# Performance work log

Measured on AMD Instinct MI355X. Metric: run time of the kernel, lower is better.

## Reference

```python
import jax, jax.numpy as jnp
import numpy as np

DIM = 512
NUM_HEADS = 16
HEAD_DIM = DIM // NUM_HEADS
HIDDEN = int(DIM * 4.0)
EPS = 1e-5


def layer_norm(x, gamma, beta):
    mu = jnp.mean(x, axis=-1, keepdims=True)
    var = jnp.mean(jnp.square(x - mu), axis=-1, keepdims=True)
    return (x - mu) * jax.lax.rsqrt(var + EPS) * gamma + beta


def setup_inputs() -> dict:
    key = jax.random.key(0)
    ks = jax.random.split(key, 8)
    B, L, C = 32, 3136, DIM
    x = jax.random.normal(ks[0], (B, L, C), dtype=jnp.float32)
    norm1_g = jnp.ones((C,), jnp.float32)
    norm1_b = jnp.zeros((C,), jnp.float32)
    # spatial (per-head) mixing weight: (num_heads, head_dim, head_dim)
    w_spatial = jax.random.normal(ks[1], (NUM_HEADS, HEAD_DIM, HEAD_DIM), jnp.float32) * (1.0 / np.sqrt(HEAD_DIM))
    norm2_g = jnp.ones((C,), jnp.float32)
    norm2_b = jnp.zeros((C,), jnp.float32)
    w1 = jax.random.normal(ks[2], (C, HIDDEN), jnp.float32) * (1.0 / np.sqrt(C))
    b1 = jnp.zeros((HIDDEN,), jnp.float32)
    w2 = jax.random.normal(ks[3], (HIDDEN, C), jnp.float32) * (1.0 / np.sqrt(HIDDEN))
    b2 = jnp.zeros((C,), jnp.float32)
    return {"x": x, "norm1_g": norm1_g, "norm1_b": norm1_b, "w_spatial": w_spatial,
            "norm2_g": norm2_g, "norm2_b": norm2_b, "w1": w1, "b1": b1, "w2": w2, "b2": b2}


def reference(x, norm1_g, norm1_b, w_spatial, norm2_g, norm2_b, w1, b1, w2, b2):
    B, L, C = x.shape
    shortcut = x
    h = layer_norm(x, norm1_g, norm1_b)
    # window partition -> per-head channel-sub-dim linear (shared across windows/positions)
    # mathematically equivalent to applying the per-head matmul at every token
    h = h.reshape(B, L, NUM_HEADS, HEAD_DIM)
    h = jnp.einsum('blhd,hde->blhe', h, w_spatial)
    h = h.reshape(B, L, C)
    x = shortcut + h
    # channel MLP: Linear -> GELU(tanh) -> Linear
    y = layer_norm(x, norm2_g, norm2_b)
    y = jax.nn.gelu(y @ w1 + b1, approximate=True)
    y = y @ w2 + b2
    return x + y
```

## Files before the change

kernel.cpp:

```cpp
#include <hip/hip_runtime.h>
#include <hip/hip_bf16.h>


typedef __bf16 bf16x8 __attribute__((ext_vector_type(8)));
typedef float f32x4 __attribute__((ext_vector_type(4)));

constexpr int CDIM = 512;
constexpr int HID = 2048;
constexpr int MROWS = 32 * 3136;
constexpr float LN_EPS = 1e-5f;

static __device__ __forceinline__ float gelu_tanh(float x) {
  const float u = 0.7978845608028654f * fmaf(0.044715f * x * x, x, x);
  const float e = __expf(2.0f * u);
  return 0.5f * x * (2.0f - 2.0f / (e + 1.0f));
}

static __device__ __forceinline__ void load_lds16(const void* g, void* l) {
  __builtin_amdgcn_global_load_lds((__attribute__((address_space(1))) void*)g,
                                   (__attribute__((address_space(3))) void*)l,
                                   16, 0, 0);
}

template <int KD, int ND>
__global__ __launch_bounds__(256) void cvt_t(const float* __restrict__ src,
                                             __hip_bfloat16* __restrict__ dst) {
  __shared__ float tl[64][65];
  const int t = threadIdx.x;
  constexpr int NTN = ND / 64;
  const int k0 = (blockIdx.x / NTN) * 64;
  const int n0 = (blockIdx.x % NTN) * 64;
  const int c4 = (t & 15) * 4;
  const int r = t >> 4;
#pragma unroll
  for (int j = 0; j < 4; ++j) {
    const int kk = r + j * 16;
    const float4 v = *(const float4*)&src[(size_t)(k0 + kk) * ND + n0 + c4];
    tl[c4 + 0][kk] = v.x;
    tl[c4 + 1][kk] = v.y;
    tl[c4 + 2][kk] = v.z;
    tl[c4 + 3][kk] = v.w;
  }
  __syncthreads();
#pragma unroll
  for (int j = 0; j < 4; ++j) {
    const int nn = r + j * 16;
    __hip_bfloat16 o[4];
#pragma unroll
    for (int c = 0; c < 4; ++c) o[c] = __float2bfloat16(tl[nn][c4 + c]);
    *(uint2*)&dst[(size_t)(n0 + nn) * KD + k0 + c4] = *(const uint2*)o;
  }
}

__global__ __launch_bounds__(256) void fused_pre(
    const float* __restrict__ x, const float* __restrict__ g1,
    const float* __restrict__ b1, const float* __restrict__ wsp,
    const float* __restrict__ g2, const float* __restrict__ b2,
    float* __restrict__ x2out, __hip_bfloat16* __restrict__ yout) {
  __shared__ float lnbuf[CDIM];
  __shared__ float red[8];

  const int t = threadIdx.x;
  const int lane = t & 63;
  const int w = t >> 6;
  const int c0 = 2 * t;
  const int hd = c0 >> 5, e0 = c0 & 31;

  float wc0[32], wc1[32];
#pragma unroll
  for (int d = 0; d < 32; ++d) {
    const float2 wv = *(const float2*)&wsp[(hd * 32 + d) * 32 + e0];
    wc0[d] = wv.x;
    wc1[d] = wv.y;
  }
  const float2 g1v = *(const float2*)&g1[c0];
  const float2 b1v = *(const float2*)&b1[c0];
  const float2 g2v = *(const float2*)&g2[c0];
  const float2 b2v = *(const float2*)&b2[c0];

  for (int r = blockIdx.x; r < MROWS; r += gridDim.x) {
    const float2 xv = *(const float2*)&x[(size_t)r * CDIM + c0];

    float s = xv.x + xv.y, ss = xv.x * xv.x + xv.y * xv.y;
#pragma unroll
    for (int off = 32; off; off >>= 1) {
      s += __shfl_down(s, off);
      ss += __shfl_down(ss, off);
    }
    if (lane == 0) { red[w * 2] = s; red[w * 2 + 1] = ss; }
    __syncthreads();
    s = red[0] + red[2] + red[4] + red[6];
    ss = red[1] + red[3] + red[5] + red[7];
    float mu = s * (1.0f / CDIM);
    float var = ss * (1.0f / CDIM) - mu * mu;
    float rs = rsqrtf(var + LN_EPS);
    lnbuf[c0] = (xv.x - mu) * rs * g1v.x + b1v.x;
    lnbuf[c0 + 1] = (xv.y - mu) * rs * g1v.y + b1v.y;
    __syncthreads();

    float h0 = 0.f, h1 = 0.f;
#pragma unroll
    for (int d = 0; d < 32; ++d) {
      const float lv = lnbuf[hd * 32 + d];
      h0 = fmaf(lv, wc0[d], h0);
      h1 = fmaf(lv, wc1[d], h1);
    }
    const float a0 = xv.x + h0, a1 = xv.y + h1;
    float2 av;
    av.x = a0;
    av.y = a1;
    *(float2*)&x2out[(size_t)r * CDIM + c0] = av;

    s = a0 + a1;
    ss = a0 * a0 + a1 * a1;
#pragma unroll
    for (int off = 32; off; off >>= 1) {
      s += __shfl_down(s, off);
      ss += __shfl_down(ss, off);
    }
    if (lane == 0) { red[w * 2] = s; red[w * 2 + 1] = ss; }
    __syncthreads();
    s = red[0] + red[2] + red[4] + red[6];
    ss = red[1] + red[3] + red[5] + red[7];
    mu = s * (1.0f / CDIM);
    var = ss * (1.0f / CDIM) - mu * mu;
    rs = rsqrtf(var + LN_EPS);
    __hip_bfloat162 yv;
    yv.x = __float2bfloat16((a0 - mu) * rs * g2v.x + b2v.x);
    yv.y = __float2bfloat16((a1 - mu) * rs * g2v.y + b2v.y);
    *(__hip_bfloat162*)&yout[(size_t)r * CDIM + c0] = yv;
    __syncthreads();
  }
}

template <int K, int N, bool GELU>
__global__ __launch_bounds__(512, 2) void gemm8p(
    const __hip_bfloat16* __restrict__ A, const __hip_bfloat16* __restrict__ Bt,
    const float* __restrict__ bias, __hip_bfloat16* __restrict__ zout,
    float* __restrict__ fout) {
  constexpr int NT = N / 256;
  constexpr int NKT = K / 32;
  __shared__ __attribute__((aligned(16))) __hip_bfloat16 lds[4][2][256 * 32];

  const int tid = threadIdx.x;
  const int lane = tid & 63;
  const int w = tid >> 6;
  const int wm = w >> 2, wn = w & 3;

  const int cpx = gridDim.x >> 3;
  const int bid = (blockIdx.x & 7) * cpx + (blockIdx.x >> 3);
  const int tm = bid / NT, tn = bid - tm * NT;
  const size_t am0 = (size_t)tm * 256;
  const int bn0 = tn * 256;

  const int r0 = tid >> 2;
  const int ks0 = (tid & 3) ^ ((tid >> 2) & 3) ^ ((tid >> 4) & 3);
  const __hip_bfloat16* aP0 = A + (am0 + r0) * K + ks0 * 8;
  const __hip_bfloat16* aP1 = aP0 + (size_t)128 * K;
  const __hip_bfloat16* bP0 = Bt + (size_t)(bn0 + r0) * K + ks0 * 8;
  const __hip_bfloat16* bP1 = bP0 + (size_t)128 * K;
  const int lo0 = (w * 64) * 8;
  const int lo1 = (512 + w * 64) * 8;

#define STAGE_A(sl, kt)                            \
  do {                                             \
    load_lds16(aP0 + (kt) * 32, &lds[sl][0][lo0]); \
    load_lds16(aP1 + (kt) * 32, &lds[sl][0][lo1]); \
  } while (0)
#define STAGE_B(sl, kt)                            \
  do {                                             \
    load_lds16(bP0 + (kt) * 32, &lds[sl][1][lo0]); \
    load_lds16(bP1 + (kt) * 32, &lds[sl][1][lo1]); \
  } while (0)

  f32x4 acc[8][4] = {};
  const int fr = lane & 15;
  const int kgs = (((lane >> 4) ^ (lane & 3) ^ ((lane >> 2) & 3))) * 8;

  STAGE_A(0, 0);
  STAGE_B(0, 0);
  STAGE_A(1, 1);
  STAGE_B(1, 1);

  for (int t = 0; t < NKT; ++t) {
    if (t + 1 < NKT)
      asm volatile("s_waitcnt vmcnt(4)" ::: "memory");
    else
      asm volatile("s_waitcnt vmcnt(0)" ::: "memory");
    __builtin_amdgcn_s_barrier();

    const int sl = t & 3;
    const int s2 = (t + 2) & 3;
    const bool pf = (t + 2) < NKT;
    const __hip_bfloat16* As = lds[sl][0];
    const __hip_bfloat16* Bs = lds[sl][1];

    if (pf) STAGE_A(s2, t + 2);
    bf16x8 bfv[4];
#pragma unroll
    for (int n = 0; n < 4; ++n)
      bfv[n] = *(const bf16x8*)(Bs + (wn * 64 + n * 16 + fr) * 32 + kgs);
    bf16x8 af[4];
#pragma unroll
    for (int m = 0; m < 4; ++m)
      af[m] = *(const bf16x8*)(As + (wm * 128 + m * 16 + fr) * 32 + kgs);
    __builtin_amdgcn_s_setprio(1);
#pragma unroll
    for (int m = 0; m < 4; ++m)
#pragma unroll
      for (int n = 0; n < 4; ++n)
        acc[m][n] = __builtin_amdgcn_mfma_f32_16x16x32_bf16(af[m], bfv[n],
                                                            acc[m][n], 0, 0, 0);
    __builtin_amdgcn_s_setprio(0);
    __builtin_amdgcn_s_barrier();

    if (pf) STAGE_B(s2, t + 2);
#pragma unroll
    for (int m = 0; m < 4; ++m)
      af[m] = *(const bf16x8*)(As + (wm * 128 + (m + 4) * 16 + fr) * 32 + kgs);
    __builtin_amdgcn_s_setprio(1);
#pragma unroll
    for (int m = 0; m < 4; ++m)
#pragma unroll
      for (int n = 0; n < 4; ++n)
        acc[m + 4][n] = __builtin_amdgcn_mfma_f32_16x16x32_bf16(
            af[m], bfv[n], acc[m + 4][n], 0, 0, 0);
    __builtin_amdgcn_s_setprio(0);
  }
#undef STAGE_A
#undef STAGE_B

  const int cr = (lane >> 4) * 4;
  const int cc = lane & 15;
  char* smb = (char*)&lds[0][0][0];

  if constexpr (GELU) {
    __syncthreads();
    __hip_bfloat16* ot = (__hip_bfloat16*)smb;
#pragma unroll
    for (int n = 0; n < 4; ++n) {
      const int col = wn * 64 + n * 16 + cc;
      const float bv = bias[bn0 + col];
#pragma unroll
      for (int m = 0; m < 8; ++m) {
        const int row = wm * 128 + m * 16 + cr;
#pragma unroll
        for (int j = 0; j < 4; ++j)
          ot[(row + j) * 256 + col] =
              __float2bfloat16(gelu_tanh(acc[m][n][j] + bv));
      }
    }
    __syncthreads();
#pragma unroll
    for (int it = 0; it < 16; ++it) {
      const int seg = it * 512 + tid;
      const int row = seg >> 5, cs = seg & 31;
      const uint4 v = *(const uint4*)(smb + seg * 16);
      *(uint4*)&zout[(am0 + row) * N + bn0 + cs * 8] = v;
    }
  } else {
    float* ot = (float*)smb;
#pragma unroll
    for (int p = 0; p < 2; ++p) {
      __syncthreads();
      if (wm == p) {
#pragma unroll
        for (int n = 0; n < 4; ++n) {
          const int col = wn * 64 + n * 16 + cc;
          const float bv = bias[bn0 + col];
#pragma unroll
          for (int m = 0; m < 8; ++m) {
            const int rl = m * 16 + cr;
#pragma unroll
            for (int j = 0; j < 4; ++j)
              ot[(rl + j) * 256 + col] = acc[m][n][j] + bv;
          }
        }
      }
      __syncthreads();
#pragma unroll
      for (int it = 0; it < 16; ++it) {
        const int seg = it * 512 + tid;
        const int row = seg >> 6, cs = seg & 63;
        const float4 lv = *(const float4*)(smb + seg * 16);
        float* gp = &fout[(am0 + p * 128 + row) * N + bn0 + cs * 4];
        float4 o = *(const float4*)gp;
        o.x += lv.x;
        o.y += lv.y;
        o.z += lv.z;
        o.w += lv.w;
        *(float4*)gp = o;
      }
    }
  }
}

extern "C" void kernel_launch(void* const* d_in, const int* in_sizes, int n_in,
                              void* d_out, int out_size, void* d_ws,
                              size_t ws_size, hipStream_t stream) {
  const float* x = (const float*)d_in[0];
  const float* n1g = (const float*)d_in[1];
  const float* n1b = (const float*)d_in[2];
  const float* wsp = (const float*)d_in[3];
  const float* n2g = (const float*)d_in[4];
  const float* n2b = (const float*)d_in[5];
  const float* w1 = (const float*)d_in[6];
  const float* b1 = (const float*)d_in[7];
  const float* w2 = (const float*)d_in[8];
  const float* b2 = (const float*)d_in[9];
  float* out = (float*)d_out;

  __hip_bfloat16* ybuf = (__hip_bfloat16*)d_ws;
  __hip_bfloat16* zbuf = ybuf + (size_t)MROWS * CDIM;
  __hip_bfloat16* w1t = zbuf + (size_t)MROWS * HID;
  __hip_bfloat16* w2t = w1t + (size_t)CDIM * HID;

  cvt_t<CDIM, HID><<<(CDIM / 64) * (HID / 64), 256, 0, stream>>>(w1, w1t);
  cvt_t<HID, CDIM><<<(HID / 64) * (CDIM / 64), 256, 0, stream>>>(w2, w2t);
  fused_pre<<<2048, 256, 0, stream>>>(x, n1g, n1b, wsp, n2g, n2b, out, ybuf);
  gemm8p<CDIM, HID, true><<<(MROWS / 256) * (HID / 256), 512, 0, stream>>>(
      ybuf, w1t, b1, zbuf, nullptr);
  gemm8p<HID, CDIM, false><<<(MROWS / 256) * (CDIM / 256), 512, 0, stream>>>(
      zbuf, w2t, b2, nullptr, out);
}
```

Measured before the change: 938.0 us.

## Software-pipeline LDS fragment loads in GEMM and process row pairs in pre-kernel

The GEMM kernel is restructured so the A/B fragments for the next k-step are read from LDS while the current MFMAs run, with barriers and vmcnt waits moved to match. The LDS XOR swizzle is removed, giving a plain row layout, and the occupancy hint in launch_bounds is dropped. The LayerNorm/spatial pre-kernel now handles two rows per iteration to halve the barrier and reduction overhead per row. The epilogue is factored into a helper. Removing the swizzle risks LDS bank conflicts, and keeping more fragments live raises register pressure.

```diff
diff --git a/kernel.cpp b/kernel.cpp
--- a/kernel.cpp
+++ b/kernel.cpp
@@ -57,8 +57,8 @@
     const float* __restrict__ b1, const float* __restrict__ wsp,
     const float* __restrict__ g2, const float* __restrict__ b2,
     float* __restrict__ x2out, __hip_bfloat16* __restrict__ yout) {
-  __shared__ float lnbuf[CDIM];
-  __shared__ float red[8];
+  __shared__ float lnbuf[2][CDIM];
+  __shared__ float red[16];
 
   const int t = threadIdx.x;
   const int lane = t & 63;
@@ -78,162 +78,107 @@
   const float2 g2v = *(const float2*)&g2[c0];
   const float2 b2v = *(const float2*)&b2[c0];
 
-  for (int r = blockIdx.x; r < MROWS; r += gridDim.x) {
-    const float2 xv = *(const float2*)&x[(size_t)r * CDIM + c0];
-
-    float s = xv.x + xv.y, ss = xv.x * xv.x + xv.y * xv.y;
+  for (int rp = blockIdx.x; rp < MROWS / 2; rp += gridDim.x) {
+    const size_t ra = (size_t)rp * 2, rb = ra + 1;
+    const float2 xa = *(const float2*)&x[ra * CDIM + c0];
+    const float2 xb = *(const float2*)&x[rb * CDIM + c0];
+
+    float sa = xa.x + xa.y, qa = xa.x * xa.x + xa.y * xa.y;
+    float sb = xb.x + xb.y, qb = xb.x * xb.x + xb.y * xb.y;
 #pragma unroll
     for (int off = 32; off; off >>= 1) {
-      s += __shfl_down(s, off);
-      ss += __shfl_down(ss, off);
-    }
-    if (lane == 0) { red[w * 2] = s; red[w * 2 + 1] = ss; }
-    __syncthreads();
-    s = red[0] + red[2] + red[4] + red[6];
-    ss = red[1] + red[3] + red[5] + red[7];
-    float mu = s * (1.0f / CDIM);
-    float var = ss * (1.0f / CDIM) - mu * mu;
-    float rs = rsqrtf(var + LN_EPS);
-    lnbuf[c0] = (xv.x - mu) * rs * g1v.x + b1v.x;
-    lnbuf[c0 + 1] = (xv.y - mu) * rs * g1v.y + b1v.y;
-    __syncthreads();
-
-    float h0 = 0.f, h1 = 0.f;
+      sa += __shfl_down(sa, off);
+      qa += __shfl_down(qa, off);
+      sb += __shfl_down(sb, off);
+      qb += __shfl_down(qb, off);
+    }
+    if (lane == 0) {
+      red[w * 4 + 0] = sa;
+      red[w * 4 + 1] = qa;
+      red[w * 4 + 2] = sb;
+      red[w * 4 + 3] = qb;
+    }
+    __syncthreads();
+    sa = red[0] + red[4] + red[8] + red[12];
+    qa = red[1] + red[5] + red[9] + red[13];
+    sb = red[2] + red[6] + red[10] + red[14];
+    qb = red[3] + red[7] + red[11] + red[15];
+    float mua = sa * (1.0f / CDIM), mub = sb * (1.0f / CDIM);
+    float rsa = rsqrtf(qa * (1.0f / CDIM) - mua * mua + LN_EPS);
+    float rsb = rsqrtf(qb * (1.0f / CDIM) - mub * mub + LN_EPS);
+    lnbuf[0][c0] = (xa.x - mua) * rsa * g1v.x + b1v.x;
+    lnbuf[0][c0 + 1] = (xa.y - mua) * rsa * g1v.y + b1v.y;
+    lnbuf[1][c0] = (xb.x - mub) * rsb * g1v.x + b1v.x;
+    lnbuf[1][c0 + 1] = (xb.y - mub) * rsb * g1v.y + b1v.y;
+    __syncthreads();
+
+    float ha0 = 0.f, ha1 = 0.f, hb0 = 0.f, hb1 = 0.f;
 #pragma unroll
     for (int d = 0; d < 32; ++d) {
-      const float lv = lnbuf[hd * 32 + d];
-      h0 = fmaf(lv, wc0[d], h0);
-      h1 = fmaf(lv, wc1[d], h1);
-    }
-    const float a0 = xv.x + h0, a1 = xv.y + h1;
+      const float la = lnbuf[0][hd * 32 + d];
+      const float lb = lnbuf[1][hd * 32 + d];
+      ha0 = fmaf(la, wc0[d], ha0);
+      ha1 = fmaf(la, wc1[d], ha1);
+      hb0 = fmaf(lb, wc0[d], hb0);
+      hb1 = fmaf(lb, wc1[d], hb1);
+    }
+    const float a0 = xa.x + ha0, a1 = xa.y + ha1;
+    const float b0 = xb.x + hb0, b1r = xb.y + hb1;
     float2 av;
     av.x = a0;
     av.y = a1;
-    *(float2*)&x2out[(size_t)r * CDIM + c0] = av;
-
-    s = a0 + a1;
-    ss = a0 * a0 + a1 * a1;
+    *(float2*)&x2out[ra * CDIM + c0] = av;
+    av.x = b0;
+    av.y = b1r;
+    *(float2*)&x2out[rb * CDIM + c0] = av;
+
+    sa = a0 + a1;
+    qa = a0 * a0 + a1 * a1;
+    sb = b0 + b1r;
+    qb = b0 * b0 + b1r * b1r;
 #pragma unroll
     for (int off = 32; off; off >>= 1) {
-      s += __shfl_down(s, off);
-      ss += __shfl_down(ss, off);
-    }
-    if (lane == 0) { red[w * 2] = s; red[w * 2 + 1] = ss; }
-    __syncthreads();
-    s = red[0] + red[2] + red[4] + red[6];
-    ss = red[1] + red[3] + red[5] + red[7];
-    mu = s * (1.0f / CDIM);
-    var = ss * (1.0f / CDIM) - mu * mu;
-    rs = rsqrtf(var + LN_EPS);
+      sa += __shfl_down(sa, off);
+      qa += __shfl_down(qa, off);
+      sb += __shfl_down(sb, off);
+      qb += __shfl_down(qb, off);
+    }
+    if (lane == 0) {
+      red[w * 4 + 0] = sa;
+      red[w * 4 + 1] = qa;
+      red[w * 4 + 2] = sb;
+      red[w * 4 + 3] = qb;
+    }
+    __syncthreads();
+    sa = red[0] + red[4] + red[8] + red[12];
+    qa = red[1] + red[5] + red[9] + red[13];
+    sb = red[2] + red[6] + red[10] + red[14];
+    qb = red[3] + red[7] + red[11] + red[15];
+    mua = sa * (1.0f / CDIM);
+    mub = sb * (1.0f / CDIM);
+    rsa = rsqrtf(qa * (1.0f / CDIM) - mua * mua + LN_EPS);
+    rsb = rsqrtf(qb * (1.0f / CDIM) - mub * mub + LN_EPS);
     __hip_bfloat162 yv;
-    yv.x = __float2bfloat16((a0 - mu) * rs * g2v.x + b2v.x);
-    yv.y = __float2bfloat16((a1 - mu) * rs * g2v.y + b2v.y);
-    *(__hip_bfloat162*)&yout[(size_t)r * CDIM + c0] = yv;
-    __syncthreads();
-  }
-}
-
-template <int K, int N, bool GELU>
-__global__ __launch_bounds__(512, 2) void gemm8p(
-    const __hip_bfloat16* __restrict__ A, const __hip_bfloat16* __restrict__ Bt,
-    const float* __restrict__ bias, __hip_bfloat16* __restrict__ zout,
-    float* __restrict__ fout) {
-  constexpr int NT = N / 256;
-  constexpr int NKT = K / 32;
-  __shared__ __attribute__((aligned(16))) __hip_bfloat16 lds[4][2][256 * 32];
-
-  const int tid = threadIdx.x;
-  const int lane = tid & 63;
-  const int w = tid >> 6;
-  const int wm = w >> 2, wn = w & 3;
-
-  const int cpx = gridDim.x >> 3;
-  const int bid = (blockIdx.x & 7) * cpx + (blockIdx.x >> 3);
-  const int tm = bid / NT, tn = bid - tm * NT;
-  const size_t am0 = (size_t)tm * 256;
-  const int bn0 = tn * 256;
-
-  const int r0 = tid >> 2;
-  const int ks0 = (tid & 3) ^ ((tid >> 2) & 3) ^ ((tid >> 4) & 3);
-  const __hip_bfloat16* aP0 = A + (am0 + r0) * K + ks0 * 8;
-  const __hip_bfloat16* aP1 = aP0 + (size_t)128 * K;
-  const __hip_bfloat16* bP0 = Bt + (size_t)(bn0 + r0) * K + ks0 * 8;
-  const __hip_bfloat16* bP1 = bP0 + (size_t)128 * K;
-  const int lo0 = (w * 64) * 8;
-  const int lo1 = (512 + w * 64) * 8;
-
-#define STAGE_A(sl, kt)                            \
-  do {                                             \
-    load_lds16(aP0 + (kt) * 32, &lds[sl][0][lo0]); \
-    load_lds16(aP1 + (kt) * 32, &lds[sl][0][lo1]); \
-  } while (0)
-#define STAGE_B(sl, kt)                            \
-  do {                                             \
-    load_lds16(bP0 + (kt) * 32, &lds[sl][1][lo0]); \
-    load_lds16(bP1 + (kt) * 32, &lds[sl][1][lo1]); \
-  } while (0)
-
-  f32x4 acc[8][4] = {};
-  const int fr = lane & 15;
-  const int kgs = (((lane >> 4) ^ (lane & 3) ^ ((lane >> 2) & 3))) * 8;
-
-  STAGE_A(0, 0);
-  STAGE_B(0, 0);
-  STAGE_A(1, 1);
-  STAGE_B(1, 1);
-
-  for (int t = 0; t < NKT; ++t) {
-    if (t + 1 < NKT)
-      asm volatile("s_waitcnt vmcnt(4)" ::: "memory");
-    else
-      asm volatile("s_waitcnt vmcnt(0)" ::: "memory");
-    __builtin_amdgcn_s_barrier();
-
-    const int sl = t & 3;
-    const int s2 = (t + 2) & 3;
-    const bool pf = (t + 2) < NKT;
-    const __hip_bfloat16* As = lds[sl][0];
-    const __hip_bfloat16* Bs = lds[sl][1];
-
-    if (pf) STAGE_A(s2, t + 2);
-    bf16x8 bfv[4];
-#pragma unroll
-    for (int n = 0; n < 4; ++n)
-      bfv[n] = *(const bf16x8*)(Bs + (wn * 64 + n * 16 + fr) * 32 + kgs);
-    bf16x8 af[4];
-#pragma unroll
-    for (int m = 0; m < 4; ++m)
-      af[m] = *(const bf16x8*)(As + (wm * 128 + m * 16 + fr) * 32 + kgs);
-    __builtin_amdgcn_s_setprio(1);
-#pragma unroll
-    for (int m = 0; m < 4; ++m)
-#pragma unroll
-      for (int n = 0; n < 4; ++n)
-        acc[m][n] = __builtin_amdgcn_mfma_f32_16x16x32_bf16(af[m], bfv[n],
-                                                            acc[m][n], 0, 0, 0);
-    __builtin_amdgcn_s_setprio(0);
-    __builtin_amdgcn_s_barrier();
-
-    if (pf) STAGE_B(s2, t + 2);
-#pragma unroll
-    for (int m = 0; m < 4; ++m)
-      af[m] = *(const bf16x8*)(As + (wm * 128 + (m + 4) * 16 + fr) * 32 + kgs);
-    __builtin_amdgcn_s_setprio(1);
-#pragma unroll
-    for (int m = 0; m < 4; ++m)
-#pragma unroll
-      for (int n = 0; n < 4; ++n)
-        acc[m + 4][n] = __builtin_amdgcn_mfma_f32_16x16x32_bf16(
-            af[m], bfv[n], acc[m + 4][n], 0, 0, 0);
-    __builtin_amdgcn_s_setprio(0);
-  }
-#undef STAGE_A
-#undef STAGE_B
-
+    yv.x = __float2bfloat16((a0 - mua) * rsa * g2v.x + b2v.x);
+    yv.y = __float2bfloat16((a1 - mua) * rsa * g2v.y + b2v.y);
+    *(__hip_bfloat162*)&yout[ra * CDIM + c0] = yv;
+    yv.x = __float2bfloat16((b0 - mub) * rsb * g2v.x + b2v.x);
+    yv.y = __float2bfloat16((b1r - mub) * rsb * g2v.y + b2v.y);
+    *(__hip_bfloat162*)&yout[rb * CDIM + c0] = yv;
+    __syncthreads();
+  }
+}
+
+template <int N, bool GELU>
+static __device__ __forceinline__ void epilogue(const f32x4 (&acc)[8][4],
+                                                char* smb, int tid, int lane,
+                                                int wm, int wn, size_t am0,
+                                                int bn0,
+                                                const float* __restrict__ bias,
+                                                __hip_bfloat16* __restrict__ zout,
+                                                float* __restrict__ fout) {
   const int cr = (lane >> 4) * 4;
   const int cc = lane & 15;
-  char* smb = (char*)&lds[0][0][0];
-
   if constexpr (GELU) {
     __syncthreads();
     __hip_bfloat16* ot = (__hip_bfloat16*)smb;
@@ -293,6 +238,126 @@
       }
     }
   }
+}
+
+template <int K, int N, bool GELU>
+__global__ __launch_bounds__(512) void gemmpp(
+    const __hip_bfloat16* __restrict__ A, const __hip_bfloat16* __restrict__ Bt,
+    const float* __restrict__ bias, __hip_bfloat16* __restrict__ zout,
+    float* __restrict__ fout) {
+  constexpr int NT = N / 256;
+  constexpr int NKT = K / 32;
+  __shared__ __attribute__((aligned(16))) __hip_bfloat16 lds[4][2][256 * 32];
+
+  const int tid = threadIdx.x;
+  const int lane = tid & 63;
+  const int w = tid >> 6;
+  const int wm = w >> 2, wn = w & 3;
+
+  const int cpx = gridDim.x >> 3;
+  const int bid = (blockIdx.x & 7) * cpx + (blockIdx.x >> 3);
+  const int tm = bid / NT, tn = bid - tm * NT;
+  const size_t am0 = (size_t)tm * 256;
+  const int bn0 = tn * 256;
+
+  const int r0 = tid >> 2;
+  const int q0 = tid & 3;
+  const __hip_bfloat16* aP0 = A + (am0 + r0) * K + q0 * 8;
+  const __hip_bfloat16* aP1 = aP0 + (size_t)128 * K;
+  const __hip_bfloat16* bP0 = Bt + (size_t)(bn0 + r0) * K + q0 * 8;
+  const __hip_bfloat16* bP1 = bP0 + (size_t)128 * K;
+  const int lo0 = (w * 64) * 8;
+  const int lo1 = (512 + w * 64) * 8;
+
+#define STAGE_A(sl, kt)                            \
+  do {                                             \
+    load_lds16(aP0 + (kt) * 32, &lds[sl][0][lo0]); \
+    load_lds16(aP1 + (kt) * 32, &lds[sl][0][lo1]); \
+  } while (0)
+#define STAGE_B(sl, kt)                            \
+  do {                                             \
+    load_lds16(bP0 + (kt) * 32, &lds[sl][1][lo0]); \
+    load_lds16(bP1 + (kt) * 32, &lds[sl][1][lo1]); \
+  } while (0)
+
+  const int fr = lane & 15;
+  const int kb = (lane >> 4) * 16;
+
+#define LD_A03(sl)                                                          \
+  do {                                                                      \
+    _Pragma("unroll") for (int m = 0; m < 4; ++m) a03[m] =                  \
+        *(const bf16x8*)((const char*)&lds[sl][0][0] +                      \
+                         (wm * 128 + m * 16 + fr) * 64 + kb);               \
+  } while (0)
+#define LD_A47(sl)                                                          \
+  do {                                                                      \
+    _Pragma("unroll") for (int m = 0; m < 4; ++m) a47[m] =                  \
+        *(const bf16x8*)((const char*)&lds[sl][0][0] +                      \
+                         (wm * 128 + (m + 4) * 16 + fr) * 64 + kb);         \
+  } while (0)
+#define LD_B(sl)                                                            \
+  do {                                                                      \
+    _Pragma("unroll") for (int n = 0; n < 4; ++n) bf[n] =                   \
+        *(const bf16x8*)((const char*)&lds[sl][1][0] +                      \
+                         (wn * 64 + n * 16 + fr) * 64 + kb);                \
+  } while (0)
+
+  f32x4 acc[8][4] = {};
+  bf16x8 a03[4], a47[4], bf[4];
+
+  STAGE_A(0, 0);
+  STAGE_B(0, 0);
+  STAGE_A(1, 1);
+  STAGE_B(1, 1);
+  asm volatile("s_waitcnt vmcnt(4)" ::: "memory");
+  __builtin_amdgcn_s_barrier();
+  LD_A03(0);
+  LD_B(0);
+
+  for (int t = 0; t < NKT; ++t) {
+    const int sl = t & 3, sl1 = (t + 1) & 3, sl2 = (t + 2) & 3;
+    const bool pf2 = (t + 2) < NKT, pf1 = (t + 1) < NKT;
+
+    if (pf2) STAGE_A(sl2, t + 2);
+    __builtin_amdgcn_s_setprio(1);
+#pragma unroll
+    for (int m = 0; m < 4; ++m)
+#pragma unroll
+      for (int n = 0; n < 4; ++n)
+        acc[m][n] = __builtin_amdgcn_mfma_f32_16x16x32_bf16(a03[m], bf[n],
+                                                            acc[m][n], 0, 0, 0);
+    __builtin_amdgcn_s_setprio(0);
+    LD_A47(sl);
+
+    if (pf2)
+      asm volatile("s_waitcnt vmcnt(2)" ::: "memory");
+    else
+      asm volatile("s_waitcnt vmcnt(0)" ::: "memory");
+    __builtin_amdgcn_s_barrier();
+
+    if (pf2) STAGE_B(sl2, t + 2);
+    __builtin_amdgcn_s_setprio(1);
+#pragma unroll
+    for (int m = 0; m < 4; ++m)
+#pragma unroll
+      for (int n = 0; n < 4; ++n)
+        acc[m + 4][n] = __builtin_amdgcn_mfma_f32_16x16x32_bf16(
+            a47[m], bf[n], acc[m + 4][n], 0, 0, 0);
+    __builtin_amdgcn_s_setprio(0);
+    if (pf1) {
+      LD_A03(sl1);
+      LD_B(sl1);
+    }
+    __builtin_amdgcn_s_barrier();
+  }
+#undef STAGE_A
+#undef STAGE_B
+#undef LD_A03
+#undef LD_A47
+#undef LD_B
+
+  epilogue<N, GELU>(acc, (char*)&lds[0][0][0], tid, lane, wm, wn, am0, bn0,
+                    bias, zout, fout);
 }
 
 extern "C" void kernel_launch(void* const* d_in, const int* in_sizes, int n_in,
@@ -318,8 +383,8 @@
   cvt_t<CDIM, HID><<<(CDIM / 64) * (HID / 64), 256, 0, stream>>>(w1, w1t);
   cvt_t<HID, CDIM><<<(HID / 64) * (CDIM / 64), 256, 0, stream>>>(w2, w2t);
   fused_pre<<<2048, 256, 0, stream>>>(x, n1g, n1b, wsp, n2g, n2b, out, ybuf);
-  gemm8p<CDIM, HID, true><<<(MROWS / 256) * (HID / 256), 512, 0, stream>>>(
+  gemmpp<CDIM, HID, true><<<(MROWS / 256) * (HID / 256), 512, 0, stream>>>(
       ybuf, w1t, b1, zbuf, nullptr);
-  gemm8p<HID, CDIM, false><<<(MROWS / 256) * (CDIM / 256), 512, 0, stream>>>(
+  gemmpp<HID, CDIM, false><<<(MROWS / 256) * (CDIM / 256), 512, 0, stream>>>(
       zbuf, w2t, b2, nullptr, out);
 }
```

Result: no change. 921.7 us (-1.7%).
